# Performance work log

Hardware: AMD Instinct MI355X
Metric: run time of the kernel (lower is better)

The kernel has to match this reference:

```python
import jax, jax.numpy as jnp
import numpy as np

N_ENTITIES = 100000
EMBED = 64
BATCH = 4096
TEMPERATURE = 0.2


def _infonce(v1, v2, temperature):
    # v1, v2: [B, d]
    B = v1.shape[0]
    sim11 = v1 @ v1.T  # [B,B]
    sim22 = v2 @ v2.T
    sim12 = v1 @ v2.T
    eye = jnp.eye(B, dtype=bool)
    neg_inf = jnp.float32(-jnp.inf)
    sim11 = jnp.where(eye, neg_inf, sim11)
    sim22 = jnp.where(eye, neg_inf, sim22)
    logits1 = jnp.concatenate([sim12, sim11], axis=-1)          # [B,2B]
    logits2 = jnp.concatenate([sim22, sim12.T], axis=-1)        # [B,2B]
    logits = jnp.concatenate([logits1, logits2], axis=0) / temperature  # [2B,2B]
    targets = jnp.arange(2 * B)
    logp = jax.nn.log_softmax(logits, axis=-1)
    return -jnp.mean(jnp.take_along_axis(logp, targets[:, None], axis=-1))


def setup_inputs() -> dict:
    key = jax.random.key(0)
    k1, k2, k3, k4, k5, k6 = jax.random.split(key, 6)
    return {
        "input_u_list": jax.random.randint(k1, (BATCH,), 0, N_ENTITIES),
        "input_i_list": jax.random.randint(k2, (BATCH,), 0, N_ENTITIES),
        "u_sub1_embeddings": jax.random.normal(k3, (N_ENTITIES, EMBED), dtype=jnp.float32),
        "i_sub1_embeddings": jax.random.normal(k4, (N_ENTITIES, EMBED), dtype=jnp.float32),
        "u_sub2_embeddings": jax.random.normal(k5, (N_ENTITIES, EMBED), dtype=jnp.float32),
        "i_sub2_embeddings": jax.random.normal(k6, (N_ENTITIES, EMBED), dtype=jnp.float32),
    }


def reference(input_u_list, input_i_list, u_sub1_embeddings, i_sub1_embeddings,
              u_sub2_embeddings, i_sub2_embeddings):
    # user branch: gather + L2-normalize
    u1 = u_sub1_embeddings[input_u_list]
    u2 = u_sub2_embeddings[input_u_list]
    u1 = u1 / jnp.linalg.norm(u1, axis=1, keepdims=True)
    u2 = u2 / jnp.linalg.norm(u2, axis=1, keepdims=True)
    user_cl_loss = _infonce(u1, u2, TEMPERATURE)
    # item branch: gather only (the original does NOT normalize items)
    i1 = i_sub1_embeddings[input_i_list]
    i2 = i_sub2_embeddings[input_i_list]
    item_cl_loss = _infonce(i1, i2, TEMPERATURE)
    return user_cl_loss + item_cl_loss
```

## Files before the change

### kernel.cpp

```cpp
#include <hip/hip_runtime.h>
#include <hip/hip_bf16.h>
#include <math.h>

#define B_SZ   4096
#define D      64
#define RPB    8192
#define NCHUNK 8
#define TPC    8
#define NPART  16
#define LN2    0.69314718055994531f
#define PRESCALE 2.6857914f

typedef __attribute__((ext_vector_type(8))) short  bf16x8;
typedef __attribute__((ext_vector_type(4))) float  f32x4;

__device__ __forceinline__ float fexp2(float x) { return __builtin_amdgcn_exp2f(x); }


__global__ __launch_bounds__(256) void gather_kernel(
    const int* __restrict__ u_idx, const int* __restrict__ i_idx,
    const float* __restrict__ u1e, const float* __restrict__ i1e,
    const float* __restrict__ u2e, const float* __restrict__ i2e,
    __hip_bfloat16* __restrict__ Xbf, float* __restrict__ dots)
{
    const int tid  = threadIdx.x;
    const int wave = tid >> 6, lane = tid & 63;
    const int g      = blockIdx.x * 4 + wave;
    const int branch = g >> 12;
    const int i      = g & (B_SZ - 1);
    const int idx    = (branch == 0) ? u_idx[i] : i_idx[i];
    const float* s1  = (branch == 0) ? u1e : i1e;
    const float* s2  = (branch == 0) ? u2e : i2e;

    float v1 = s1[(size_t)idx * D + lane];
    float v2 = s2[(size_t)idx * D + lane];
    if (branch == 0) {
        float a = v1 * v1, b = v2 * v2;
        #pragma unroll
        for (int o = 32; o > 0; o >>= 1) {
            a += __shfl_xor(a, o, 64);
            b += __shfl_xor(b, o, 64);
        }
        v1 *= rsqrtf(a);
        v2 *= rsqrtf(b);
    }
    float p = v1 * v2;
    #pragma unroll
    for (int o = 32; o > 0; o >>= 1) p += __shfl_xor(p, o, 64);
    if (lane == 0) dots[g] = p;

    const size_t row1 = (size_t)branch * RPB + i;
    Xbf[row1 * D + lane]          = __float2bfloat16(v1 * PRESCALE);
    Xbf[(row1 + B_SZ) * D + lane] = __float2bfloat16(v2 * PRESCALE);
}

template<int IS_USER>
__device__ __forceinline__ void gram_body(
    const __hip_bfloat16* __restrict__ Xb, float2* __restrict__ P,
    __hip_bfloat16 (&Bs)[128][72], int bx, int chunk, int tid)
{
    const int r0   = bx * 128;
    const int wave = tid >> 6, lane = tid & 63;
    const int wm = wave >> 1, wn = wave & 1;
    const int quad = lane >> 4, tx = lane & 15;

    #pragma unroll
    for (int p = 0; p < 4; ++p) {
        int e = p * 256 + tid;
        int row = e >> 3, c8 = e & 7;
        *(uint4*)&Bs[row][c8 * 8] =
            *(const uint4*)(Xb + (size_t)(r0 + row) * D + c8 * 8);
    }
    __syncthreads();
    bf16x8 afr[4][2];
    #pragma unroll
    for (int mt = 0; mt < 4; ++mt)
        #pragma unroll
        for (int ks = 0; ks < 2; ++ks)
            afr[mt][ks] = *(const bf16x8*)&Bs[wm * 64 + mt * 16 + tx][ks * 32 + quad * 8];

    float m_run[16], s_run[16];
    #pragma unroll
    for (int r = 0; r < 16; ++r) { m_run[r] = -INFINITY; s_run[r] = 0.f; }

    const int lrq  = wm * 64 + quad * 4;
    const int lcol = wn * 64 + tx;

    for (int t = 0; t < TPC; ++t) {
        const int ct = chunk * TPC + t;
        const int c0 = ct * 128;
        __syncthreads();
        #pragma unroll
        for (int p = 0; p < 4; ++p) {
            int e = p * 256 + tid;
            int row = e >> 3, c8 = e & 7;
            *(uint4*)&Bs[row][c8 * 8] =
                *(const uint4*)(Xb + (size_t)(c0 + row) * D + c8 * 8);
        }
        __syncthreads();

        f32x4 acc[4][4];
        const f32x4 z = {0.f, 0.f, 0.f, 0.f};
        #pragma unroll
        for (int nt = 0; nt < 4; ++nt) {
            const bf16x8 b0 = *(const bf16x8*)&Bs[wn * 64 + nt * 16 + tx][quad * 8];
            #pragma unroll
            for (int mt = 0; mt < 4; ++mt)
                acc[mt][nt] = __builtin_amdgcn_mfma_f32_16x16x32_bf16(afr[mt][0], b0, z, 0, 0, 0);
        }
        #pragma unroll
        for (int nt = 0; nt < 4; ++nt) {
            const bf16x8 b1 = *(const bf16x8*)&Bs[wn * 64 + nt * 16 + tx][32 + quad * 8];
            #pragma unroll
            for (int mt = 0; mt < 4; ++mt)
                acc[mt][nt] = __builtin_amdgcn_mfma_f32_16x16x32_bf16(afr[mt][1], b1, acc[mt][nt], 0, 0, 0);
        }

        const bool diag = (ct == bx);
        #pragma unroll
        for (int mt = 0; mt < 4; ++mt) {
            #pragma unroll
            for (int rr = 0; rr < 4; ++rr) {
                float y0 = acc[mt][0][rr], y1 = acc[mt][1][rr],
                      y2 = acc[mt][2][rr], y3 = acc[mt][3][rr];
                if (diag) {
                    const int dr = lrq + mt * 16 + rr - lcol;
                    if (dr == 0)  y0 = -INFINITY;
                    if (dr == 16) y1 = -INFINITY;
                    if (dr == 32) y2 = -INFINITY;
                    if (dr == 48) y3 = -INFINITY;
                }
                const int r = mt * 4 + rr;
                if (IS_USER) {
                    s_run[r] += fexp2(y0) + fexp2(y1) + fexp2(y2) + fexp2(y3);
                } else {
                    float mx   = fmaxf(fmaxf(y0, y1), fmaxf(y2, y3));
                    float newm = fmaxf(m_run[r], mx);
                    s_run[r] = s_run[r] * fexp2(m_run[r] - newm)
                             + fexp2(y0 - newm) + fexp2(y1 - newm)
                             + fexp2(y2 - newm) + fexp2(y3 - newm);
                    m_run[r] = newm;
                }
            }
        }
    }

    #pragma unroll
    for (int r = 0; r < 16; ++r) {
        float m = IS_USER ? 0.f : m_run[r];
        float s = s_run[r];
        #pragma unroll
        for (int o = 1; o < 16; o <<= 1) {
            if (IS_USER) {
                s += __shfl_xor(s, o, 64);
            } else {
                float om = __shfl_xor(m, o, 64);
                float os = __shfl_xor(s, o, 64);
                float M  = fmaxf(m, om);
                s = s * fexp2(m - M) + os * fexp2(om - M);
                m = M;
            }
        }
        if (tx == 0) {
            const int grow = r0 + wm * 64 + (r >> 2) * 16 + quad * 4 + (r & 3);
            P[(size_t)grow * NPART + chunk * 2 + wn] = make_float2(m, s);
        }
    }
}

__global__ __launch_bounds__(256, 4) void gram_lse_kernel(
    const __hip_bfloat16* __restrict__ Xbf, float2* __restrict__ P)
{
    __shared__ __align__(16) __hip_bfloat16 Bs[128][72];
    const int chunk = blockIdx.x, bx = blockIdx.y, bz = blockIdx.z;
    if (bz == 0)
        gram_body<1>(Xbf, P, Bs, bx, chunk, threadIdx.x);
    else
        gram_body<0>(Xbf + (size_t)RPB * D, P + (size_t)RPB * NPART,
                     Bs, bx, chunk, threadIdx.x);
}

__global__ __launch_bounds__(256) void merge_kernel(
    const float2* __restrict__ P, const float* __restrict__ dots,
    float* __restrict__ out)
{
    __shared__ float red[4];
    const int tid  = threadIdx.x;
    const int wave = tid >> 6, lane = tid & 63;
    const int gw   = blockIdx.x * 4 + wave;
    const int row  = gw * 4 + (lane >> 4);
    const int c    = lane & 15;

    float2 p = P[(size_t)row * NPART + c];
    float m = p.x, s = p.y;
    #pragma unroll
    for (int o = 1; o < 16; o <<= 1) {
        float om = __shfl_xor(m, o, 64);
        float os = __shfl_xor(s, o, 64);
        float M  = fmaxf(m, om);
        s = s * fexp2(m - M) + os * fexp2(om - M);
        m = M;
    }

    float v = 0.f;
    if ((lane & 15) == 0)
        v = LN2 * (m + log2f(s)) * (1.0f / (float)RPB);
    if (tid < 8)
        v -= dots[blockIdx.x * 8 + tid] * (5.0f / (float)B_SZ);

    #pragma unroll
    for (int o = 32; o > 0; o >>= 1) v += __shfl_xor(v, o, 64);
    if (lane == 0) red[wave] = v;
    __syncthreads();
    if (tid == 0)
        atomicAdd(out, red[0] + red[1] + red[2] + red[3]);
}

extern "C" void kernel_launch(void* const* d_in, const int* in_sizes, int n_in,
                              void* d_out, int out_size, void* d_ws, size_t ws_size,
                              hipStream_t stream) {
    const int*   u_idx = (const int*)d_in[0];
    const int*   i_idx = (const int*)d_in[1];
    const float* u1e   = (const float*)d_in[2];
    const float* i1e   = (const float*)d_in[3];
    const float* u2e   = (const float*)d_in[4];
    const float* i2e   = (const float*)d_in[5];
    float* out = (float*)d_out;

    __hip_bfloat16* Xbf = (__hip_bfloat16*)d_ws;
    float*  dots = (float*)((char*)d_ws + 2 * RPB * D * 2);
    float2* P    = (float2*)((char*)dots + RPB * sizeof(float));

    hipMemsetAsync(out, 0, sizeof(float), stream);

    gather_kernel<<<dim3(2048), dim3(256), 0, stream>>>(
        u_idx, i_idx, u1e, i1e, u2e, i2e, Xbf, dots);
    gram_lse_kernel<<<dim3(NCHUNK, 64, 2), dim3(256), 0, stream>>>(Xbf, P);
    merge_kernel<<<dim3(1024), dim3(256), 0, stream>>>(P, dots, out);
}
```

Measured before the change: 203.9 us.

## Replace LDS-tiled gram with per-wave register-fed strips and direct global loads

```diff
diff --git a/kernel.cpp b/kernel.cpp
--- a/kernel.cpp
+++ b/kernel.cpp
@@ -6,8 +6,7 @@
 #define D      64
 #define RPB    8192
 #define NCHUNK 8
-#define TPC    8
-#define NPART  16
+#define TPW    16
 #define LN2    0.69314718055994531f
 #define PRESCALE 2.6857914f
 
@@ -57,78 +56,76 @@
 template<int IS_USER>
 __device__ __forceinline__ void gram_body(
     const __hip_bfloat16* __restrict__ Xb, float2* __restrict__ P,
-    __hip_bfloat16 (&Bs)[128][72], int bx, int chunk, int tid)
-{
-    const int r0   = bx * 128;
-    const int wave = tid >> 6, lane = tid & 63;
-    const int wm = wave >> 1, wn = wave & 1;
+    int strip, int chunk, int lane)
+{
     const int quad = lane >> 4, tx = lane & 15;
-
-    #pragma unroll
-    for (int p = 0; p < 4; ++p) {
-        int e = p * 256 + tid;
-        int row = e >> 3, c8 = e & 7;
-        *(uint4*)&Bs[row][c8 * 8] =
-            *(const uint4*)(Xb + (size_t)(r0 + row) * D + c8 * 8);
-    }
-    __syncthreads();
-    bf16x8 afr[4][2];
-    #pragma unroll
-    for (int mt = 0; mt < 4; ++mt)
+    const int r0   = strip * 32;
+    const int voff = tx * D + quad * 8;
+
+    bf16x8 afr[2][2];
+    {
+        const __hip_bfloat16* pa = Xb + (size_t)r0 * D + voff;
+        #pragma unroll
+        for (int mt = 0; mt < 2; ++mt)
+            #pragma unroll
+            for (int ks = 0; ks < 2; ++ks)
+                afr[mt][ks] = *(const bf16x8*)(pa + mt * 16 * D + ks * 32);
+    }
+
+    float m_run[8], s_run[8];
+    #pragma unroll
+    for (int r = 0; r < 8; ++r) { m_run[r] = -INFINITY; s_run[r] = 0.f; }
+
+    const int c0_0 = chunk * TPW * 64;
+    const __hip_bfloat16* pb = Xb + (size_t)c0_0 * D + voff;
+
+    bf16x8 bfr[4][2];
+    #pragma unroll
+    for (int nt = 0; nt < 4; ++nt)
         #pragma unroll
         for (int ks = 0; ks < 2; ++ks)
-            afr[mt][ks] = *(const bf16x8*)&Bs[wm * 64 + mt * 16 + tx][ks * 32 + quad * 8];
-
-    float m_run[16], s_run[16];
-    #pragma unroll
-    for (int r = 0; r < 16; ++r) { m_run[r] = -INFINITY; s_run[r] = 0.f; }
-
-    const int lrq  = wm * 64 + quad * 4;
-    const int lcol = wn * 64 + tx;
-
-    for (int t = 0; t < TPC; ++t) {
-        const int ct = chunk * TPC + t;
-        const int c0 = ct * 128;
-        __syncthreads();
-        #pragma unroll
-        for (int p = 0; p < 4; ++p) {
-            int e = p * 256 + tid;
-            int row = e >> 3, c8 = e & 7;
-            *(uint4*)&Bs[row][c8 * 8] =
-                *(const uint4*)(Xb + (size_t)(c0 + row) * D + c8 * 8);
-        }
-        __syncthreads();
-
-        f32x4 acc[4][4];
+            bfr[nt][ks] = *(const bf16x8*)(pb + nt * 16 * D + ks * 32);
+
+    for (int t = 0; t < TPW; ++t) {
+        const int c0 = c0_0 + t * 64;
+
+        f32x4 acc[2][4];
         const f32x4 z = {0.f, 0.f, 0.f, 0.f};
         #pragma unroll
-        for (int nt = 0; nt < 4; ++nt) {
-            const bf16x8 b0 = *(const bf16x8*)&Bs[wn * 64 + nt * 16 + tx][quad * 8];
-            #pragma unroll
-            for (int mt = 0; mt < 4; ++mt)
-                acc[mt][nt] = __builtin_amdgcn_mfma_f32_16x16x32_bf16(afr[mt][0], b0, z, 0, 0, 0);
-        }
-        #pragma unroll
-        for (int nt = 0; nt < 4; ++nt) {
-            const bf16x8 b1 = *(const bf16x8*)&Bs[wn * 64 + nt * 16 + tx][32 + quad * 8];
-            #pragma unroll
-            for (int mt = 0; mt < 4; ++mt)
-                acc[mt][nt] = __builtin_amdgcn_mfma_f32_16x16x32_bf16(afr[mt][1], b1, acc[mt][nt], 0, 0, 0);
-        }
-
-        const bool diag = (ct == bx);
-        #pragma unroll
-        for (int mt = 0; mt < 4; ++mt) {
+        for (int nt = 0; nt < 4; ++nt)
+            #pragma unroll
+            for (int mt = 0; mt < 2; ++mt)
+                acc[mt][nt] = __builtin_amdgcn_mfma_f32_16x16x32_bf16(
+                    afr[mt][0], bfr[nt][0], z, 0, 0, 0);
+        #pragma unroll
+        for (int nt = 0; nt < 4; ++nt)
+            #pragma unroll
+            for (int mt = 0; mt < 2; ++mt)
+                acc[mt][nt] = __builtin_amdgcn_mfma_f32_16x16x32_bf16(
+                    afr[mt][1], bfr[nt][1], acc[mt][nt], 0, 0, 0);
+
+        if (t + 1 < TPW) {
+            const __hip_bfloat16* pn = pb + (size_t)(t + 1) * 64 * D;
+            #pragma unroll
+            for (int nt = 0; nt < 4; ++nt)
+                #pragma unroll
+                for (int ks = 0; ks < 2; ++ks)
+                    bfr[nt][ks] = *(const bf16x8*)(pn + nt * 16 * D + ks * 32);
+        }
+
+        const bool diag = (r0 >= c0) && (r0 < c0 + 64);
+        #pragma unroll
+        for (int mt = 0; mt < 2; ++mt) {
             #pragma unroll
             for (int rr = 0; rr < 4; ++rr) {
                 float y0 = acc[mt][0][rr], y1 = acc[mt][1][rr],
                       y2 = acc[mt][2][rr], y3 = acc[mt][3][rr];
                 if (diag) {
-                    const int dr = lrq + mt * 16 + rr - lcol;
-                    if (dr == 0)  y0 = -INFINITY;
-                    if (dr == 16) y1 = -INFINITY;
-                    if (dr == 32) y2 = -INFINITY;
-                    if (dr == 48) y3 = -INFINITY;
+                    const int dd = (r0 - c0) + mt * 16 + quad * 4 + rr - tx;
+                    if (dd == 0)  y0 = -INFINITY;
+                    if (dd == 16) y1 = -INFINITY;
+                    if (dd == 32) y2 = -INFINITY;
+                    if (dd == 48) y3 = -INFINITY;
                 }
                 const int r = mt * 4 + rr;
                 if (IS_USER) {
@@ -146,7 +143,7 @@
     }
 
     #pragma unroll
-    for (int r = 0; r < 16; ++r) {
+    for (int r = 0; r < 8; ++r) {
         float m = IS_USER ? 0.f : m_run[r];
         float s = s_run[r];
         #pragma unroll
@@ -162,22 +159,24 @@
             }
         }
         if (tx == 0) {
-            const int grow = r0 + wm * 64 + (r >> 2) * 16 + quad * 4 + (r & 3);
-            P[(size_t)grow * NPART + chunk * 2 + wn] = make_float2(m, s);
-        }
-    }
-}
-
-__global__ __launch_bounds__(256, 4) void gram_lse_kernel(
+            const int row = r0 + (r >> 2) * 16 + quad * 4 + (r & 3);
+            P[(size_t)row * NCHUNK + chunk] = make_float2(m, s);
+        }
+    }
+}
+
+__global__ __launch_bounds__(256, 4) void gram_kernel(
     const __hip_bfloat16* __restrict__ Xbf, float2* __restrict__ P)
 {
-    __shared__ __align__(16) __hip_bfloat16 Bs[128][72];
-    const int chunk = blockIdx.x, bx = blockIdx.y, bz = blockIdx.z;
-    if (bz == 0)
-        gram_body<1>(Xbf, P, Bs, bx, chunk, threadIdx.x);
+    const int tid  = threadIdx.x;
+    const int wave = tid >> 6, lane = tid & 63;
+    const int strip = blockIdx.y * 4 + wave;
+    const int chunk = blockIdx.x;
+    if (blockIdx.z == 0)
+        gram_body<1>(Xbf, P, strip, chunk, lane);
     else
-        gram_body<0>(Xbf + (size_t)RPB * D, P + (size_t)RPB * NPART,
-                     Bs, bx, chunk, threadIdx.x);
+        gram_body<0>(Xbf + (size_t)RPB * D, P + (size_t)RPB * NCHUNK,
+                     strip, chunk, lane);
 }
 
 __global__ __launch_bounds__(256) void merge_kernel(
@@ -187,14 +186,13 @@
     __shared__ float red[4];
     const int tid  = threadIdx.x;
     const int wave = tid >> 6, lane = tid & 63;
-    const int gw   = blockIdx.x * 4 + wave;
-    const int row  = gw * 4 + (lane >> 4);
-    const int c    = lane & 15;
-
-    float2 p = P[(size_t)row * NPART + c];
+    const int row  = (blockIdx.x * 4 + wave) * 8 + (lane >> 3);
+    const int c    = lane & 7;
+
+    float2 p = P[(size_t)row * NCHUNK + c];
     float m = p.x, s = p.y;
     #pragma unroll
-    for (int o = 1; o < 16; o <<= 1) {
+    for (int o = 1; o < 8; o <<= 1) {
         float om = __shfl_xor(m, o, 64);
         float os = __shfl_xor(s, o, 64);
         float M  = fmaxf(m, om);
@@ -203,10 +201,10 @@
     }
 
     float v = 0.f;
-    if ((lane & 15) == 0)
+    if ((lane & 7) == 0)
         v = LN2 * (m + log2f(s)) * (1.0f / (float)RPB);
-    if (tid < 8)
-        v -= dots[blockIdx.x * 8 + tid] * (5.0f / (float)B_SZ);
+    if (tid < 16)
+        v -= dots[blockIdx.x * 16 + tid] * (5.0f / (float)B_SZ);
 
     #pragma unroll
     for (int o = 32; o > 0; o >>= 1) v += __shfl_xor(v, o, 64);
@@ -235,6 +233,6 @@
 
     gather_kernel<<<dim3(2048), dim3(256), 0, stream>>>(
         u_idx, i_idx, u1e, i1e, u2e, i2e, Xbf, dots);
-    gram_lse_kernel<<<dim3(NCHUNK, 64, 2), dim3(256), 0, stream>>>(Xbf, P);
-    merge_kernel<<<dim3(1024), dim3(256), 0, stream>>>(P, dots, out);
-}
+    gram_kernel<<<dim3(NCHUNK, 64, 2), dim3(256), 0, stream>>>(Xbf, P);
+    merge_kernel<<<dim3(512), dim3(256), 0, stream>>>(P, dots, out);
+}
```

Measured after the change: 189.9 us. 6.9% less time.
